# Optimization experiments

Hardware: AMD Instinct MI355X
Metric: run time of the kernel (lower is better)

Reference implementation:

```python
import jax, jax.numpy as jnp
import numpy as np

B, S, D_IN, D_H, D_OUT = 8, 4096, 512, 1024, 512


def setup_inputs() -> dict:
    key = jax.random.key(0)
    ks = jax.random.split(key, 7)
    # scale weights by 1/sqrt(fan_in) so activations stay O(1) through the ReLU stack
    return {
        "query": jax.random.normal(ks[0], (B, S, D_IN), dtype=jnp.float32),
        "W0": jax.random.normal(ks[1], (B, D_H, D_IN), dtype=jnp.float32) * (D_IN ** -0.5),
        "b0": jax.random.normal(ks[2], (B, D_H), dtype=jnp.float32) * 0.02,
        "W1": jax.random.normal(ks[3], (B, D_H, D_H), dtype=jnp.float32) * (D_H ** -0.5),
        "b1": jax.random.normal(ks[4], (B, D_H), dtype=jnp.float32) * 0.02,
        "W2": jax.random.normal(ks[5], (B, D_OUT, D_H), dtype=jnp.float32) * (D_H ** -0.5),
        "b2": jax.random.normal(ks[6], (B, D_OUT), dtype=jnp.float32) * 0.02,
    }


def reference(query, W0, b0, W1, b1, W2, b2):
    # Original loops over (seq, batch) issuing F.linear per sample with per-batch
    # weights; this is exactly a batched GEMM over the batch axis.
    # F.linear(x, w, b) = x @ w.T + b, with w[b] of shape [out, in].
    h = jax.nn.relu(jnp.einsum('bsd,bhd->bsh', query, W0) + b0[:, None, :])  # [B,S,H]
    h = jax.nn.relu(jnp.einsum('bsh,bgh->bsg', h, W1) + b1[:, None, :])      # [B,S,H]
    out = jnp.einsum('bsg,bog->bso', h, W2) + b2[:, None, :]                 # [B,S,O]
    return out
```

## Files before the change

### kernel.cpp

```cpp
#include <hip/hip_runtime.h>


typedef _Float16 f16x8 __attribute__((ext_vector_type(8)));
typedef _Float16 f16x4 __attribute__((ext_vector_type(4)));
typedef float    f32x4 __attribute__((ext_vector_type(4)));

__device__ __forceinline__ void stage16(const void* g, void* l) {
    __builtin_amdgcn_global_load_lds(
        (const __attribute__((address_space(1))) unsigned int*)g,
        (__attribute__((address_space(3))) unsigned int*)l,
        16, 0, 0);
}

__device__ __forceinline__ void cast_seg(const float* __restrict__ s,
                                         _Float16* __restrict__ d, int n4) {
    const int stride = gridDim.x * 256;
    for (int i = blockIdx.x * 256 + threadIdx.x; i < n4; i += stride) {
        float4 f = reinterpret_cast<const float4*>(s)[i];
        f16x4 o;
        o[0] = (_Float16)f.x; o[1] = (_Float16)f.y;
        o[2] = (_Float16)f.z; o[3] = (_Float16)f.w;
        reinterpret_cast<f16x4*>(d)[i] = o;
    }
}

__global__ __launch_bounds__(256) void cast_all(
    const float* s0, _Float16* d0, int n0,
    const float* s1, _Float16* d1, int n1,
    const float* s2, _Float16* d2, int n2,
    const float* s3, _Float16* d3, int n3) {
    cast_seg(s0, d0, n0);
    cast_seg(s1, d1, n1);
    cast_seg(s2, d2, n2);
    cast_seg(s3, d3, n3);
}

template <bool RELU, bool OUT_F16>
__global__ __launch_bounds__(256) void gemm_dbuf(
    const _Float16* __restrict__ A, const _Float16* __restrict__ W,
    const float* __restrict__ bias, void* __restrict__ Outv,
    int M, int N, int K) {
    constexpr int BM = 128, BN = 128, BK = 32;
    __shared__ __align__(16) _Float16 As[2][BM * BK];
    __shared__ __align__(16) _Float16 Bs[2][BN * BK];

    const int tid  = threadIdx.x;
    const int lane = tid & 63;
    const int rowl = lane & 15;
    const int q8   = (lane >> 4) * 8;
    const int wm   = ((tid >> 6) >> 1) * 64;
    const int wn   = ((tid >> 6) & 1) * 64;

    const int bm = blockIdx.x, bn = blockIdx.y, b = blockIdx.z;

    const int c0 = tid, c1 = tid + 256;
    const int ar0 = c0 >> 2, ak0 = (c0 & 3) * 8;
    const int ar1 = c1 >> 2, ak1 = (c1 & 3) * 8;

    const char* Ab = (const char*)(A + (size_t)b * M * K + (size_t)(bm * BM) * K);
    const char* Wb = (const char*)(W + (size_t)b * N * K + (size_t)(bn * BN) * K);
    size_t aoff0 = ((size_t)ar0 * K + ak0) * 2;
    size_t aoff1 = ((size_t)ar1 * K + ak1) * 2;
    size_t woff0 = ((size_t)ar0 * K + ak0) * 2;
    size_t woff1 = ((size_t)ar1 * K + ak1) * 2;

    f32x4 acc[4][4];
#pragma unroll
    for (int mi = 0; mi < 4; ++mi)
#pragma unroll
        for (int ni = 0; ni < 4; ++ni)
            acc[mi][ni] = (f32x4){0.f, 0.f, 0.f, 0.f};

    stage16(Ab + aoff0, &As[0][8 * (size_t)c0]);
    stage16(Ab + aoff1, &As[0][8 * (size_t)c1]);
    stage16(Wb + woff0, &Bs[0][8 * (size_t)c0]);
    stage16(Wb + woff1, &Bs[0][8 * (size_t)c1]);
    aoff0 += BK * 2; aoff1 += BK * 2; woff0 += BK * 2; woff1 += BK * 2;

    const int nk = K / BK;
    for (int kk = 0; kk < nk; ++kk) {
        const int cur = kk & 1;
        __syncthreads();
        if (kk + 1 < nk) {
            const int nxt = cur ^ 1;
            stage16(Ab + aoff0, &As[nxt][8 * (size_t)c0]);
            stage16(Ab + aoff1, &As[nxt][8 * (size_t)c1]);
            stage16(Wb + woff0, &Bs[nxt][8 * (size_t)c0]);
            stage16(Wb + woff1, &Bs[nxt][8 * (size_t)c1]);
            aoff0 += BK * 2; aoff1 += BK * 2; woff0 += BK * 2; woff1 += BK * 2;
        }

        f16x8 af[4], bf[4];
#pragma unroll
        for (int i = 0; i < 4; ++i)
            af[i] = *(const f16x8*)(&As[cur][(wm + i * 16 + rowl) * BK + q8]);
#pragma unroll
        for (int i = 0; i < 4; ++i)
            bf[i] = *(const f16x8*)(&Bs[cur][(wn + i * 16 + rowl) * BK + q8]);
#pragma unroll
        for (int mi = 0; mi < 4; ++mi)
#pragma unroll
            for (int ni = 0; ni < 4; ++ni)
                acc[mi][ni] = __builtin_amdgcn_mfma_f32_16x16x32_f16(
                    af[mi], bf[ni], acc[mi][ni], 0, 0, 0);
    }

    const int q = lane >> 4;
    float bcol[4];
    {
        const float* bp = bias + (size_t)b * N + bn * BN + wn;
#pragma unroll
        for (int ni = 0; ni < 4; ++ni) bcol[ni] = bp[ni * 16 + rowl];
    }
#pragma unroll
    for (int mi = 0; mi < 4; ++mi) {
        const int row0 = bm * BM + wm + mi * 16 + q * 4;
#pragma unroll
        for (int r = 0; r < 4; ++r) {
            const size_t ro = (size_t)b * M * N + (size_t)(row0 + r) * N + bn * BN + wn;
#pragma unroll
            for (int ni = 0; ni < 4; ++ni) {
                float v = acc[mi][ni][r] + bcol[ni];
                if (RELU) v = fmaxf(v, 0.f);
                if (OUT_F16)
                    ((_Float16*)Outv)[ro + ni * 16 + rowl] = (_Float16)v;
                else
                    ((float*)Outv)[ro + ni * 16 + rowl] = v;
            }
        }
    }
}

__device__ __forceinline__ uint4 load8f32(const char* p) {
    const float4* fp = reinterpret_cast<const float4*>(p);
    float4 f0 = fp[0], f1 = fp[1];
    f16x8 o;
    o[0] = (_Float16)f0.x; o[1] = (_Float16)f0.y;
    o[2] = (_Float16)f0.z; o[3] = (_Float16)f0.w;
    o[4] = (_Float16)f1.x; o[5] = (_Float16)f1.y;
    o[6] = (_Float16)f1.z; o[7] = (_Float16)f1.w;
    return __builtin_bit_cast(uint4, o);
}

template <bool A_F16, bool W_F16, bool RELU, bool OUT_F16>
__global__ __launch_bounds__(256) void gemm_bias_act(
    const void* __restrict__ Av, const void* __restrict__ Wv,
    const float* __restrict__ bias, void* __restrict__ Outv,
    int M, int N, int K) {
    constexpr int BM = 128, BN = 128, BK = 32;
    __shared__ __align__(16) _Float16 As[BM * BK];
    __shared__ __align__(16) _Float16 Bs[BN * BK];

    const int tid  = threadIdx.x;
    const int lane = tid & 63;
    const int rowl = lane & 15;
    const int q8   = (lane >> 4) * 8;
    const int wm   = ((tid >> 6) >> 1) * 64;
    const int wn   = ((tid >> 6) & 1) * 64;
    const int bm = blockIdx.x, bn = blockIdx.y, b = blockIdx.z;

    const int c0 = tid, c1 = tid + 256;
    const int ar0 = c0 >> 2, ak0 = (c0 & 3) * 8;
    const int ar1 = c1 >> 2, ak1 = (c1 & 3) * 8;

    constexpr size_t esA = A_F16 ? 2 : 4;
    constexpr size_t esW = W_F16 ? 2 : 4;
    const char* Abase = (const char*)Av;
    const char* Wbase = (const char*)Wv;

    size_t aoff0 = ((size_t)b * M * K + (size_t)(bm * BM + ar0) * K + ak0) * esA;
    size_t aoff1 = ((size_t)b * M * K + (size_t)(bm * BM + ar1) * K + ak1) * esA;
    size_t woff0 = ((size_t)b * N * K + (size_t)(bn * BN + ar0) * K + ak0) * esW;
    size_t woff1 = ((size_t)b * N * K + (size_t)(bn * BN + ar1) * K + ak1) * esW;

    f32x4 acc[4][4];
#pragma unroll
    for (int mi = 0; mi < 4; ++mi)
#pragma unroll
        for (int ni = 0; ni < 4; ++ni)
            acc[mi][ni] = (f32x4){0.f, 0.f, 0.f, 0.f};

    const int nk = K / BK;
    for (int kk = 0; kk < nk; ++kk) {
        uint4 va0, va1, vw0, vw1;
        if (!A_F16) { va0 = load8f32(Abase + aoff0); va1 = load8f32(Abase + aoff1); }
        if (!W_F16) { vw0 = load8f32(Wbase + woff0); vw1 = load8f32(Wbase + woff1); }
        __syncthreads();
        if (A_F16) {
            stage16(Abase + aoff0, As + 8 * (size_t)c0);
            stage16(Abase + aoff1, As + 8 * (size_t)c1);
        } else {
            *(uint4*)(As + ar0 * BK + ak0) = va0;
            *(uint4*)(As + ar1 * BK + ak1) = va1;
        }
        if (W_F16) {
            stage16(Wbase + woff0, Bs + 8 * (size_t)c0);
            stage16(Wbase + woff1, Bs + 8 * (size_t)c1);
        } else {
            *(uint4*)(Bs + ar0 * BK + ak0) = vw0;
            *(uint4*)(Bs + ar1 * BK + ak1) = vw1;
        }
        aoff0 += BK * esA; aoff1 += BK * esA;
        woff0 += BK * esW; woff1 += BK * esW;
        __syncthreads();

        f16x8 af[4], bf[4];
#pragma unroll
        for (int i = 0; i < 4; ++i)
            af[i] = *(const f16x8*)(As + (wm + i * 16 + rowl) * BK + q8);
#pragma unroll
        for (int i = 0; i < 4; ++i)
            bf[i] = *(const f16x8*)(Bs + (wn + i * 16 + rowl) * BK + q8);
#pragma unroll
        for (int mi = 0; mi < 4; ++mi)
#pragma unroll
            for (int ni = 0; ni < 4; ++ni)
                acc[mi][ni] = __builtin_amdgcn_mfma_f32_16x16x32_f16(
                    af[mi], bf[ni], acc[mi][ni], 0, 0, 0);
    }

    const int q = lane >> 4;
    float bcol[4];
    {
        const float* bp = bias + (size_t)b * N + bn * BN + wn;
#pragma unroll
        for (int ni = 0; ni < 4; ++ni) bcol[ni] = bp[ni * 16 + rowl];
    }
#pragma unroll
    for (int mi = 0; mi < 4; ++mi) {
        const int row0 = bm * BM + wm + mi * 16 + q * 4;
#pragma unroll
        for (int r = 0; r < 4; ++r) {
            const size_t ro = (size_t)b * M * N + (size_t)(row0 + r) * N + bn * BN + wn;
#pragma unroll
            for (int ni = 0; ni < 4; ++ni) {
                float v = acc[mi][ni][r] + bcol[ni];
                if (RELU) v = fmaxf(v, 0.f);
                if (OUT_F16)
                    ((_Float16*)Outv)[ro + ni * 16 + rowl] = (_Float16)v;
                else
                    ((float*)Outv)[ro + ni * 16 + rowl] = v;
            }
        }
    }
}

extern "C" void kernel_launch(void* const* d_in, const int* in_sizes, int n_in,
                              void* d_out, int out_size, void* d_ws, size_t ws_size,
                              hipStream_t stream) {
    const int B = 8, S = 4096, DI = 512, DH = 1024, DO = 512;
    const float* query = (const float*)d_in[0];
    const float* W0    = (const float*)d_in[1];
    const float* b0    = (const float*)d_in[2];
    const float* W1    = (const float*)d_in[3];
    const float* b1    = (const float*)d_in[4];
    const float* W2    = (const float*)d_in[5];
    const float* b2    = (const float*)d_in[6];

    char* ws = (char*)d_ws;
    const size_t nH  = (size_t)B * S * DH;
    const size_t nQ  = (size_t)B * S * DI;
    const size_t nW0 = (size_t)B * DH * DI;
    const size_t nW1 = (size_t)B * DH * DH;
    const size_t nW2 = (size_t)B * DO * DH;

    _Float16* h0 = (_Float16*)ws;
    _Float16* h1 = (_Float16*)(ws + nH * 2);
    const size_t off_casts = nH * 4;
    const size_t full_need = off_casts + (nQ + nW0 + nW1 + nW2) * 2;

    const dim3 blk(256);
    const dim3 g0(S / 128, DH / 128, B);
    const dim3 g2(S / 128, DO / 128, B);

    if (ws_size >= full_need) {
        _Float16* qf  = (_Float16*)(ws + off_casts);
        _Float16* w0f = qf + nQ;
        _Float16* w1f = w0f + nW0;
        _Float16* w2f = w1f + nW1;
        cast_all<<<dim3(2048), blk, 0, stream>>>(
            query, qf, (int)(nQ / 4), W0, w0f, (int)(nW0 / 4),
            W1, w1f, (int)(nW1 / 4), W2, w2f, (int)(nW2 / 4));
        gemm_dbuf<true,  true ><<<g0, blk, 0, stream>>>(qf, w0f, b0, h0, S, DH, DI);
        gemm_dbuf<true,  true ><<<g0, blk, 0, stream>>>(h0, w1f, b1, h1, S, DH, DH);
        gemm_dbuf<false, false><<<g2, blk, 0, stream>>>(h1, w2f, b2, d_out, S, DO, DH);
    } else {
        gemm_bias_act<false, false, true,  true ><<<g0, blk, 0, stream>>>(query, W0, b0, h0, S, DH, DI);
        gemm_bias_act<true,  false, true,  true ><<<g0, blk, 0, stream>>>(h0, W1, b1, h1, S, DH, DH);
        gemm_bias_act<true,  false, false, false><<<g2, blk, 0, stream>>>(h1, W2, b2, d_out, S, DO, DH);
    }
}
```

Measured before the change: 365.3 us.

## Use 256x256 tiles with 4-stage LDS pipeline and MFMA priority boost

Replaces the double-buffered 128x128 GEMM with a 512-thread 256x256 tile kernel using a 4-deep global-to-LDS ring with explicit vmcnt waits and a single barrier per k-step. Wave priority is raised around the MFMA block. Aims to increase operand reuse per LDS load and hide global latency; costs large LDS footprint (one block per CU) and fewer blocks for tail balance.

```diff
diff --git a/kernel.cpp b/kernel.cpp
--- a/kernel.cpp
+++ b/kernel.cpp
@@ -36,24 +36,26 @@
 }
 
 template <bool RELU, bool OUT_F16>
-__global__ __launch_bounds__(256) void gemm_dbuf(
+__global__ __launch_bounds__(512, 2) void gemm_pipe(
     const _Float16* __restrict__ A, const _Float16* __restrict__ W,
     const float* __restrict__ bias, void* __restrict__ Outv,
     int M, int N, int K) {
-    constexpr int BM = 128, BN = 128, BK = 32;
-    __shared__ __align__(16) _Float16 As[2][BM * BK];
-    __shared__ __align__(16) _Float16 Bs[2][BN * BK];
+    constexpr int BM = 256, BN = 256, BK = 32;
+    constexpr int DEPTH = 4;
+    __shared__ __align__(16) _Float16 As[DEPTH][BM * BK];
+    __shared__ __align__(16) _Float16 Bs[DEPTH][BN * BK];
 
     const int tid  = threadIdx.x;
     const int lane = tid & 63;
     const int rowl = lane & 15;
     const int q8   = (lane >> 4) * 8;
-    const int wm   = ((tid >> 6) >> 1) * 64;
-    const int wn   = ((tid >> 6) & 1) * 64;
+    const int w    = tid >> 6;
+    const int wm   = (w >> 2) * 128;
+    const int wn   = (w & 3) * 64;
 
     const int bm = blockIdx.x, bn = blockIdx.y, b = blockIdx.z;
 
-    const int c0 = tid, c1 = tid + 256;
+    const int c0 = tid, c1 = tid + 512;
     const int ar0 = c0 >> 2, ak0 = (c0 & 3) * 8;
     const int ar1 = c1 >> 2, ak1 = (c1 & 3) * 8;
 
@@ -63,46 +65,67 @@
     size_t aoff1 = ((size_t)ar1 * K + ak1) * 2;
     size_t woff0 = ((size_t)ar0 * K + ak0) * 2;
     size_t woff1 = ((size_t)ar1 * K + ak1) * 2;
-
-    f32x4 acc[4][4];
-#pragma unroll
-    for (int mi = 0; mi < 4; ++mi)
+    constexpr size_t KSTEP = (size_t)BK * 2;
+
+    f32x4 acc[8][4];
+#pragma unroll
+    for (int mi = 0; mi < 8; ++mi)
 #pragma unroll
         for (int ni = 0; ni < 4; ++ni)
             acc[mi][ni] = (f32x4){0.f, 0.f, 0.f, 0.f};
 
-    stage16(Ab + aoff0, &As[0][8 * (size_t)c0]);
-    stage16(Ab + aoff1, &As[0][8 * (size_t)c1]);
-    stage16(Wb + woff0, &Bs[0][8 * (size_t)c0]);
-    stage16(Wb + woff1, &Bs[0][8 * (size_t)c1]);
-    aoff0 += BK * 2; aoff1 += BK * 2; woff0 += BK * 2; woff1 += BK * 2;
-
     const int nk = K / BK;
-    for (int kk = 0; kk < nk; ++kk) {
-        const int cur = kk & 1;
-        __syncthreads();
-        if (kk + 1 < nk) {
-            const int nxt = cur ^ 1;
+
+#pragma unroll
+    for (int p = 0; p < DEPTH - 1; ++p) {
+        if (p < nk) {
+            stage16(Ab + aoff0, &As[p][8 * (size_t)c0]);
+            stage16(Ab + aoff1, &As[p][8 * (size_t)c1]);
+            stage16(Wb + woff0, &Bs[p][8 * (size_t)c0]);
+            stage16(Wb + woff1, &Bs[p][8 * (size_t)c1]);
+            aoff0 += KSTEP; aoff1 += KSTEP; woff0 += KSTEP; woff1 += KSTEP;
+        }
+    }
+    asm volatile("s_waitcnt vmcnt(8)" ::: "memory");
+    __builtin_amdgcn_s_barrier();
+
+    for (int t = 0; t < nk; ++t) {
+        const int cur = t & (DEPTH - 1);
+        if (t + 3 < nk) {
+            const int nxt = (t + 3) & (DEPTH - 1);
             stage16(Ab + aoff0, &As[nxt][8 * (size_t)c0]);
             stage16(Ab + aoff1, &As[nxt][8 * (size_t)c1]);
             stage16(Wb + woff0, &Bs[nxt][8 * (size_t)c0]);
             stage16(Wb + woff1, &Bs[nxt][8 * (size_t)c1]);
-            aoff0 += BK * 2; aoff1 += BK * 2; woff0 += BK * 2; woff1 += BK * 2;
-        }
-
-        f16x8 af[4], bf[4];
-#pragma unroll
-        for (int i = 0; i < 4; ++i)
+            aoff0 += KSTEP; aoff1 += KSTEP; woff0 += KSTEP; woff1 += KSTEP;
+        }
+
+        f16x8 af[8], bf[4];
+#pragma unroll
+        for (int i = 0; i < 8; ++i)
             af[i] = *(const f16x8*)(&As[cur][(wm + i * 16 + rowl) * BK + q8]);
 #pragma unroll
         for (int i = 0; i < 4; ++i)
             bf[i] = *(const f16x8*)(&Bs[cur][(wn + i * 16 + rowl) * BK + q8]);
-#pragma unroll
-        for (int mi = 0; mi < 4; ++mi)
+
+        __builtin_amdgcn_s_setprio(1);
+#pragma unroll
+        for (int mi = 0; mi < 8; ++mi)
 #pragma unroll
             for (int ni = 0; ni < 4; ++ni)
                 acc[mi][ni] = __builtin_amdgcn_mfma_f32_16x16x32_f16(
                     af[mi], bf[ni], acc[mi][ni], 0, 0, 0);
+        __builtin_amdgcn_s_setprio(0);
+
+        if (t + 1 < nk) {
+            if (t + 3 < nk)
+                asm volatile("s_waitcnt vmcnt(8)" ::: "memory");
+            else if (t + 2 < nk)
+                asm volatile("s_waitcnt vmcnt(4)" ::: "memory");
+            else
+                asm volatile("s_waitcnt vmcnt(0)" ::: "memory");
+            __builtin_amdgcn_s_barrier();
+        }
     }
 
     const int q = lane >> 4;
@@ -113,7 +136,7 @@
         for (int ni = 0; ni < 4; ++ni) bcol[ni] = bp[ni * 16 + rowl];
     }
 #pragma unroll
-    for (int mi = 0; mi < 4; ++mi) {
+    for (int mi = 0; mi < 8; ++mi) {
         const int row0 = bm * BM + wm + mi * 16 + q * 4;
 #pragma unroll
         for (int r = 0; r < 4; ++r) {
@@ -269,22 +292,24 @@
     const size_t off_casts = nH * 4;
     const size_t full_need = off_casts + (nQ + nW0 + nW1 + nW2) * 2;
 
-    const dim3 blk(256);
-    const dim3 g0(S / 128, DH / 128, B);
-    const dim3 g2(S / 128, DO / 128, B);
-
     if (ws_size >= full_need) {
         _Float16* qf  = (_Float16*)(ws + off_casts);
         _Float16* w0f = qf + nQ;
         _Float16* w1f = w0f + nW0;
         _Float16* w2f = w1f + nW1;
-        cast_all<<<dim3(2048), blk, 0, stream>>>(
+        cast_all<<<dim3(2048), dim3(256), 0, stream>>>(
             query, qf, (int)(nQ / 4), W0, w0f, (int)(nW0 / 4),
             W1, w1f, (int)(nW1 / 4), W2, w2f, (int)(nW2 / 4));
-        gemm_dbuf<true,  true ><<<g0, blk, 0, stream>>>(qf, w0f, b0, h0, S, DH, DI);
-        gemm_dbuf<true,  true ><<<g0, blk, 0, stream>>>(h0, w1f, b1, h1, S, DH, DH);
-        gemm_dbuf<false, false><<<g2, blk, 0, stream>>>(h1, w2f, b2, d_out, S, DO, DH);
+        const dim3 blk(512);
+        const dim3 g0(S / 256, DH / 256, B);
+        const dim3 g2(S / 256, DO / 256, B);
+        gemm_pipe<true,  true ><<<g0, blk, 0, stream>>>(qf, w0f, b0, h0, S, DH, DI);
+        gemm_pipe<true,  true ><<<g0, blk, 0, stream>>>(h0, w1f, b1, h1, S, DH, DH);
+        gemm_pipe<false, false><<<g2, blk, 0, stream>>>(h1, w2f, b2, d_out, S, DO, DH);
     } else {
+        const dim3 blk(256);
+        const dim3 g0(S / 128, DH / 128, B);
+        const dim3 g2(S / 128, DO / 128, B);
         gemm_bias_act<false, false, true,  true ><<<g0, blk, 0, stream>>>(query, W0, b0, h0, S, DH, DI);
         gemm_bias_act<true,  false, true,  true ><<<g0, blk, 0, stream>>>(h0, W1, b1, h1, S, DH, DH);
         gemm_bias_act<true,  false, false, false><<<g2, blk, 0, stream>>>(h1, W2, b2, d_out, S, DO, DH);
```

Measured after the change: 366.2 us. Within noise of the previous version (+0.3%).
